# Performance work log

Measured on AMD Instinct MI355X. Metric: run time of the kernel, lower is better.

Reference implementation:

```python
import jax, jax.numpy as jnp
import numpy as np

B, T, E = 8, 1024, 1024
H, HS = 16, 64  # num_heads, head_size; H*HS == E


def setup_inputs() -> dict:
    key = jax.random.key(0)
    k1, k2, k3, k4, k5, k6 = jax.random.split(key, 6)
    x = jax.random.normal(k1, (B, T, E), dtype=jnp.float32)
    s = E ** -0.5
    Wk = jax.random.normal(k2, (H, HS, E), dtype=jnp.float32) * s
    Wq = jax.random.normal(k3, (H, HS, E), dtype=jnp.float32) * s
    Wv = jax.random.normal(k4, (H, HS, E), dtype=jnp.float32) * s
    Wproj = jax.random.normal(k5, (E, E), dtype=jnp.float32) * s
    i = 0
    return {"x": x, "Wk": Wk, "Wq": Wq, "Wv": Wv, "Wproj": Wproj, "i": i}


def reference(x, Wk, Wq, Wv, Wproj, i):
    # choices fixed at full supernet config: embed_dim=E, head_size=HS, no biases.
    b, t, e = x.shape
    hs = Wk.shape[1]
    # per-head projections, heads batched: [B,H,T,HS]
    k = jnp.einsum('bte,hde->bhtd', x, Wk)
    q = jnp.einsum('bte,hde->bhtd', x, Wq)
    v = jnp.einsum('bte,hde->bhtd', x, Wv)
    wei = jnp.einsum('bhtd,bhsd->bhts', q, k) * (hs ** -0.5)  # [B,H,T,T]
    causal = jnp.tril(jnp.ones((t, t), dtype=bool))
    wei = jnp.where(causal, wei, -jnp.inf)
    wei = jax.nn.softmax(wei, axis=-1)  # dropout p=0 (eval)
    out = jnp.einsum('bhts,bhsd->bthd', wei, v).reshape(b, t, -1)  # concat heads
    out = out @ Wproj.T  # proj, bias_proj=False
    return out
```

## Files before the change

### kernel.cpp

```cpp
#include <hip/hip_runtime.h>

#define B_  8
#define T_  1024
#define E_  1024
#define H_  16
#define HS_ 64
#define K_  1024

typedef __bf16 bf16x8 __attribute__((ext_vector_type(8)));
typedef float  f32x4  __attribute__((ext_vector_type(4)));
typedef unsigned short us;

__device__ __forceinline__ us f2bf(float f) {
    union { float f; unsigned int i; } c; c.f = f;
    unsigned int x = c.i;
    return (us)((x + 0x7fff + ((x >> 16) & 1)) >> 16);
}
__device__ __forceinline__ us f2bf_t(float f) {
    union { float f; unsigned int i; } c; c.f = f;
    return (us)(c.i >> 16);
}
__device__ __forceinline__ bf16x8 cvt8(const float* p) {
    float4 a = *reinterpret_cast<const float4*>(p);
    float4 b = *reinterpret_cast<const float4*>(p + 4);
    union { bf16x8 v; us u[8]; } c;
    c.u[0] = f2bf(a.x); c.u[1] = f2bf(a.y); c.u[2] = f2bf(a.z); c.u[3] = f2bf(a.w);
    c.u[4] = f2bf(b.x); c.u[5] = f2bf(b.y); c.u[6] = f2bf(b.z); c.u[7] = f2bf(b.w);
    return c.v;
}
__device__ __forceinline__ void async_cp16(const us* g, us* l) {
    __builtin_amdgcn_global_load_lds((const unsigned int*)g, (unsigned int*)l, 16, 0, 0);
}

__global__ __launch_bounds__(256) void cvt_kernel(
    const float* __restrict__ sx, const float* __restrict__ sq,
    const float* __restrict__ sk, const float* __restrict__ sv,
    const float* __restrict__ sp,
    us* __restrict__ dx, us* __restrict__ dq, us* __restrict__ dk,
    us* __restrict__ dv, us* __restrict__ dp)
{
    const int y = blockIdx.y;
    const float* src = (y == 0) ? sx : (y == 1) ? sq : (y == 2) ? sk : (y == 3) ? sv : sp;
    us*          dst = (y == 0) ? dx : (y == 1) ? dq : (y == 2) ? dk : (y == 3) ? dv : dp;
    const size_t n = (y == 0) ? (size_t)B_ * T_ * E_ : (size_t)E_ * E_;
    const size_t i = ((size_t)blockIdx.x * 256 + threadIdx.x) * 8;
    if (i >= n) return;
    *reinterpret_cast<bf16x8*>(dst + i) = cvt8(src + i);
}

__global__ __launch_bounds__(256) void qkv_gf(
    const us* __restrict__ A,
    const us* __restrict__ Wq, const us* __restrict__ Wk, const us* __restrict__ Wv,
    us* __restrict__ q, us* __restrict__ k, us* __restrict__ vT)
{
    const int type = blockIdx.z;
    const us* Bm = (type == 0) ? Wq : (type == 1) ? Wk : Wv;
    us* out      = (type == 0) ? q  : (type == 1) ? k  : vT;
    const int vtrans = (type == 2);

    __shared__ __align__(16) us As[128 * 64];
    __shared__ __align__(16) us Bs[128 * 64];

    const int tid  = threadIdx.x;
    const int lane = tid & 63;
    const int w    = tid >> 6;
    const int quad = lane >> 4;
    const int l15  = lane & 15;
    const int wm   = w >> 1, wn = w & 1;
    const int row0 = blockIdx.x * 128;
    const int col0 = blockIdx.y * 128;
    const int x7   = l15 & 7;

    f32x4 acc[4][4] = {};
    for (int k0 = 0; k0 < K_; k0 += 64) {
        __syncthreads();
#pragma unroll
        for (int i = 0; i < 4; ++i) {
            const int idx = tid + i * 256;
            const int r   = idx >> 3;
            const int c8  = ((idx & 7) ^ (r & 7)) * 8;
            async_cp16(A  + (size_t)(row0 + r) * K_ + k0 + c8, &As[idx * 8]);
            async_cp16(Bm + (size_t)(col0 + r) * K_ + k0 + c8, &Bs[idx * 8]);
        }
        __syncthreads();
#pragma unroll
        for (int kk = 0; kk < 2; ++kk) {
            const int ca = ((kk * 4 + quad) ^ x7) * 8;
            bf16x8 af[4], bf[4];
#pragma unroll
            for (int t = 0; t < 4; ++t) {
                af[t] = *reinterpret_cast<const bf16x8*>(&As[(wm * 64 + t * 16 + l15) * 64 + ca]);
                bf[t] = *reinterpret_cast<const bf16x8*>(&Bs[(wn * 64 + t * 16 + l15) * 64 + ca]);
            }
#pragma unroll
            for (int mt = 0; mt < 4; ++mt)
#pragma unroll
                for (int nt = 0; nt < 4; ++nt)
                    acc[mt][nt] = __builtin_amdgcn_mfma_f32_16x16x32_bf16(af[mt], bf[nt], acc[mt][nt], 0, 0, 0);
        }
    }

#pragma unroll
    for (int mt = 0; mt < 4; ++mt)
#pragma unroll
        for (int nt = 0; nt < 4; ++nt)
#pragma unroll
            for (int r = 0; r < 4; ++r) {
                const int m = row0 + wm * 64 + mt * 16 + quad * 4 + r;
                const int n = col0 + wn * 64 + nt * 16 + l15;
                const int b = m >> 10, t = m & 1023;
                const int h = n >> 6,  d = n & 63;
                const us vb = f2bf(acc[mt][nt][r]);
                if (vtrans)  out[((size_t)((b * 16 + h) * 64 + d)) * 1024 + t] = vb;
                else         out[((size_t)(b * 16 + h) * 1024 + t) * 64 + d] = vb;
            }
}

__global__ __launch_bounds__(256) void proj_gf(
    const us* __restrict__ A, const us* __restrict__ Bm, float* __restrict__ C)
{
    __shared__ __align__(16) us As[128 * 64];
    __shared__ __align__(16) us Bs[128 * 64];

    const int tid  = threadIdx.x;
    const int lane = tid & 63;
    const int w    = tid >> 6;
    const int quad = lane >> 4;
    const int l15  = lane & 15;
    const int wm   = w >> 1, wn = w & 1;
    const int row0 = blockIdx.x * 128;
    const int col0 = blockIdx.y * 128;
    const int x7   = l15 & 7;

    f32x4 acc[4][4] = {};
    for (int k0 = 0; k0 < K_; k0 += 64) {
        __syncthreads();
#pragma unroll
        for (int i = 0; i < 4; ++i) {
            const int idx = tid + i * 256;
            const int r   = idx >> 3;
            const int c8  = ((idx & 7) ^ (r & 7)) * 8;
            async_cp16(A  + (size_t)(row0 + r) * K_ + k0 + c8, &As[idx * 8]);
            async_cp16(Bm + (size_t)(col0 + r) * K_ + k0 + c8, &Bs[idx * 8]);
        }
        __syncthreads();
#pragma unroll
        for (int kk = 0; kk < 2; ++kk) {
            const int ca = ((kk * 4 + quad) ^ x7) * 8;
            bf16x8 af[4], bf[4];
#pragma unroll
            for (int t = 0; t < 4; ++t) {
                af[t] = *reinterpret_cast<const bf16x8*>(&As[(wm * 64 + t * 16 + l15) * 64 + ca]);
                bf[t] = *reinterpret_cast<const bf16x8*>(&Bs[(wn * 64 + t * 16 + l15) * 64 + ca]);
            }
#pragma unroll
            for (int mt = 0; mt < 4; ++mt)
#pragma unroll
                for (int nt = 0; nt < 4; ++nt)
                    acc[mt][nt] = __builtin_amdgcn_mfma_f32_16x16x32_bf16(af[mt], bf[nt], acc[mt][nt], 0, 0, 0);
        }
    }

#pragma unroll
    for (int mt = 0; mt < 4; ++mt)
#pragma unroll
        for (int nt = 0; nt < 4; ++nt)
#pragma unroll
            for (int r = 0; r < 4; ++r) {
                const int m = row0 + wm * 64 + mt * 16 + quad * 4 + r;
                const int n = col0 + wn * 64 + nt * 16 + l15;
                C[(size_t)m * E_ + n] = acc[mt][nt][r];
            }
}

#define CSCALE 0.18033688011112042f

__device__ __forceinline__ void qk_step_nomax(
    const us (*kt)[72], us (*psw)[72],
    const bf16x8& qf0, const bf16x8& qf1,
    float* lsum,
    int s0, int rowlo, int quad, int l15, bool diag)
{
    f32x4 sacc[4] = {};
#pragma unroll
    for (int nt = 0; nt < 4; ++nt) {
        bf16x8 kf0 = *reinterpret_cast<const bf16x8*>(&kt[nt * 16 + l15][quad * 8]);
        bf16x8 kf1 = *reinterpret_cast<const bf16x8*>(&kt[nt * 16 + l15][quad * 8 + 32]);
        sacc[nt] = __builtin_amdgcn_mfma_f32_16x16x32_bf16(qf0, kf0, sacc[nt], 0, 0, 0);
        sacc[nt] = __builtin_amdgcn_mfma_f32_16x16x32_bf16(qf1, kf1, sacc[nt], 0, 0, 0);
    }
    if (diag) {
#pragma unroll
        for (int nt = 0; nt < 4; ++nt)
#pragma unroll
            for (int r = 0; r < 4; ++r)
                if (s0 + nt * 16 + l15 > rowlo + quad * 4 + r) sacc[nt][r] = -1e30f;
    }
#pragma unroll
    for (int r = 0; r < 4; ++r)
#pragma unroll
        for (int nt = 0; nt < 4; ++nt) {
            const float p = exp2f(sacc[nt][r] * CSCALE);
            lsum[r] += p;
            psw[quad * 4 + r][nt * 16 + l15] = f2bf_t(p);
        }
}

__global__ __launch_bounds__(256) void attn_v6(
    const us* __restrict__ Q, const us* __restrict__ K,
    const us* __restrict__ VT, us* __restrict__ O)
{
    const int px = blockIdx.x;
    const int bh = blockIdx.y;
    const int tA = px, tB = 15 - px;
    const size_t base  = (size_t)bh * T_ * HS_;
    const size_t baseT = (size_t)bh * HS_ * T_;
    const int tid  = threadIdx.x;
    const int w    = tid >> 6;
    const int lane = tid & 63;
    const int quad = lane >> 4;
    const int l15  = lane & 15;

    __shared__ __align__(16) us kt[64][72];
    __shared__ __align__(16) us vt[64][72];
    __shared__ __align__(16) us psA[4][16][72];
    __shared__ __align__(16) us psB[4][16][72];

    const int rowA = tA * 64 + w * 16;
    const int rowB = tB * 64 + w * 16;

    bf16x8 qfA0, qfA1, qfB0, qfB1;
    {
        const us* qa = Q + base + (size_t)(rowA + l15) * HS_ + quad * 8;
        const us* qb = Q + base + (size_t)(rowB + l15) * HS_ + quad * 8;
        qfA0 = *reinterpret_cast<const bf16x8*>(qa);
        qfA1 = *reinterpret_cast<const bf16x8*>(qa + 32);
        qfB0 = *reinterpret_cast<const bf16x8*>(qb);
        qfB1 = *reinterpret_cast<const bf16x8*>(qb + 32);
    }

    float lA[4] = {0.f, 0.f, 0.f, 0.f}, lB[4] = {0.f, 0.f, 0.f, 0.f};
    f32x4 oA[4] = {}, oB[4] = {};

    const int nch = tB + 1;
    for (int ch = 0; ch < nch; ++ch) {
        const int s0 = ch * 64;
        __syncthreads();
#pragma unroll
        for (int i = 0; i < 2; ++i) {
            const int idx = tid + i * 256;
            const int r   = idx >> 3;
            const int c8  = (idx & 7) * 8;
            *reinterpret_cast<bf16x8*>(&kt[r][c8]) =
                *reinterpret_cast<const bf16x8*>(K + base + (size_t)(s0 + r) * HS_ + c8);
            *reinterpret_cast<bf16x8*>(&vt[r][c8]) =
                *reinterpret_cast<const bf16x8*>(VT + baseT + (size_t)r * T_ + s0 + c8);
        }
        __syncthreads();

        const bool actA = (ch <= tA);
        qk_step_nomax(kt, psB[w], qfB0, qfB1, lB, s0, rowB, quad, l15, ch == tB);
        if (actA)
            qk_step_nomax(kt, psA[w], qfA0, qfA1, lA, s0, rowA, quad, l15, ch == tA);

        bf16x8 pfB0 = *reinterpret_cast<const bf16x8*>(&psB[w][l15][quad * 8]);
        bf16x8 pfB1 = *reinterpret_cast<const bf16x8*>(&psB[w][l15][quad * 8 + 32]);
        bf16x8 pfA0, pfA1;
        if (actA) {
            pfA0 = *reinterpret_cast<const bf16x8*>(&psA[w][l15][quad * 8]);
            pfA1 = *reinterpret_cast<const bf16x8*>(&psA[w][l15][quad * 8 + 32]);
        }
#pragma unroll
        for (int dt = 0; dt < 4; ++dt) {
            bf16x8 vf0 = *reinterpret_cast<const bf16x8*>(&vt[dt * 16 + l15][quad * 8]);
            bf16x8 vf1 = *reinterpret_cast<const bf16x8*>(&vt[dt * 16 + l15][quad * 8 + 32]);
            oB[dt] = __builtin_amdgcn_mfma_f32_16x16x32_bf16(pfB0, vf0, oB[dt], 0, 0, 0);
            oB[dt] = __builtin_amdgcn_mfma_f32_16x16x32_bf16(pfB1, vf1, oB[dt], 0, 0, 0);
            if (actA) {
                oA[dt] = __builtin_amdgcn_mfma_f32_16x16x32_bf16(pfA0, vf0, oA[dt], 0, 0, 0);
                oA[dt] = __builtin_amdgcn_mfma_f32_16x16x32_bf16(pfA1, vf1, oA[dt], 0, 0, 0);
            }
        }
    }

#pragma unroll
    for (int r = 0; r < 4; ++r) {
#pragma unroll
        for (int off = 1; off < 16; off <<= 1) {
            lA[r] += __shfl_xor(lA[r], off);
            lB[r] += __shfl_xor(lB[r], off);
        }
    }
    const int b = bh >> 4, h = bh & 15;
#pragma unroll
    for (int r = 0; r < 4; ++r) {
        const float invA = 1.f / lA[r];
        const float invB = 1.f / lB[r];
        const size_t offA = ((size_t)b * T_ + rowA + quad * 4 + r) * E_ + h * HS_;
        const size_t offB = ((size_t)b * T_ + rowB + quad * 4 + r) * E_ + h * HS_;
#pragma unroll
        for (int dt = 0; dt < 4; ++dt) {
            O[offA + dt * 16 + l15] = f2bf(oA[dt][r] * invA);
            O[offB + dt * 16 + l15] = f2bf(oB[dt][r] * invB);
        }
    }
}

extern "C" void kernel_launch(void* const* d_in, const int* in_sizes, int n_in,
                              void* d_out, int out_size, void* d_ws, size_t ws_size,
                              hipStream_t stream) {
    const float* x  = (const float*)d_in[0];
    const float* Wk = (const float*)d_in[1];
    const float* Wq = (const float*)d_in[2];
    const float* Wv = (const float*)d_in[3];
    const float* Wp = (const float*)d_in[4];

    const size_t qe = (size_t)B_ * H_ * T_ * HS_;
    const size_t we = (size_t)E_ * E_;

    us* xb = (us*)d_ws;
    us* wq = xb + qe;
    us* wk = wq + we;
    us* wv = wk + we;
    us* wp = wv + we;
    us* q  = wp + we;
    us* k  = q + qe;
    us* vT = k + qe;
    us* o  = xb;

    cvt_kernel<<<dim3(4096, 5), 256, 0, stream>>>(x, Wq, Wk, Wv, Wp,
                                                  xb, wq, wk, wv, wp);
    qkv_gf<<<dim3(64, 8, 3), 256, 0, stream>>>(xb, wq, wk, wv, q, k, vT);
    attn_v6<<<dim3(8, 128), 256, 0, stream>>>(q, k, vT, o);
    proj_gf<<<dim3(64, 8), 256, 0, stream>>>(o, wp, (float*)d_out);
}
```

Baseline: 255.2 us.

## Load K and V fragments directly from global memory, dropping LDS staging and barriers

The attention kernel no longer stages each 64-row K and V^T chunk through shared memory behind two block-wide barriers. Each wave now reads its MFMA operand fragments straight from global memory, relying on L1/L2 to absorb the reuse across the four waves. The QK step is also inlined so a single K fragment load feeds both the A and B query tiles. This removes the __syncthreads stalls and LDS traffic, but adds redundant global/cache reads (each wave fetches the full K/V chunk) and exposes memory latency without any explicit prefetch.

```diff
diff --git a/kernel.cpp b/kernel.cpp
--- a/kernel.cpp
+++ b/kernel.cpp
@@ -175,38 +175,7 @@
 
 #define CSCALE 0.18033688011112042f
 
-__device__ __forceinline__ void qk_step_nomax(
-    const us (*kt)[72], us (*psw)[72],
-    const bf16x8& qf0, const bf16x8& qf1,
-    float* lsum,
-    int s0, int rowlo, int quad, int l15, bool diag)
-{
-    f32x4 sacc[4] = {};
-#pragma unroll
-    for (int nt = 0; nt < 4; ++nt) {
-        bf16x8 kf0 = *reinterpret_cast<const bf16x8*>(&kt[nt * 16 + l15][quad * 8]);
-        bf16x8 kf1 = *reinterpret_cast<const bf16x8*>(&kt[nt * 16 + l15][quad * 8 + 32]);
-        sacc[nt] = __builtin_amdgcn_mfma_f32_16x16x32_bf16(qf0, kf0, sacc[nt], 0, 0, 0);
-        sacc[nt] = __builtin_amdgcn_mfma_f32_16x16x32_bf16(qf1, kf1, sacc[nt], 0, 0, 0);
-    }
-    if (diag) {
-#pragma unroll
-        for (int nt = 0; nt < 4; ++nt)
-#pragma unroll
-            for (int r = 0; r < 4; ++r)
-                if (s0 + nt * 16 + l15 > rowlo + quad * 4 + r) sacc[nt][r] = -1e30f;
-    }
-#pragma unroll
-    for (int r = 0; r < 4; ++r)
-#pragma unroll
-        for (int nt = 0; nt < 4; ++nt) {
-            const float p = exp2f(sacc[nt][r] * CSCALE);
-            lsum[r] += p;
-            psw[quad * 4 + r][nt * 16 + l15] = f2bf_t(p);
-        }
-}
-
-__global__ __launch_bounds__(256) void attn_v6(
+__global__ __launch_bounds__(256) void attn_v7(
     const us* __restrict__ Q, const us* __restrict__ K,
     const us* __restrict__ VT, us* __restrict__ O)
 {
@@ -221,8 +190,6 @@
     const int quad = lane >> 4;
     const int l15  = lane & 15;
 
-    __shared__ __align__(16) us kt[64][72];
-    __shared__ __align__(16) us vt[64][72];
     __shared__ __align__(16) us psA[4][16][72];
     __shared__ __align__(16) us psB[4][16][72];
 
@@ -245,23 +212,54 @@
     const int nch = tB + 1;
     for (int ch = 0; ch < nch; ++ch) {
         const int s0 = ch * 64;
-        __syncthreads();
-#pragma unroll
-        for (int i = 0; i < 2; ++i) {
-            const int idx = tid + i * 256;
-            const int r   = idx >> 3;
-            const int c8  = (idx & 7) * 8;
-            *reinterpret_cast<bf16x8*>(&kt[r][c8]) =
-                *reinterpret_cast<const bf16x8*>(K + base + (size_t)(s0 + r) * HS_ + c8);
-            *reinterpret_cast<bf16x8*>(&vt[r][c8]) =
-                *reinterpret_cast<const bf16x8*>(VT + baseT + (size_t)r * T_ + s0 + c8);
-        }
-        __syncthreads();
-
         const bool actA = (ch <= tA);
-        qk_step_nomax(kt, psB[w], qfB0, qfB1, lB, s0, rowB, quad, l15, ch == tB);
-        if (actA)
-            qk_step_nomax(kt, psA[w], qfA0, qfA1, lA, s0, rowA, quad, l15, ch == tA);
+
+        f32x4 sA[4] = {}, sB[4] = {};
+#pragma unroll
+        for (int nt = 0; nt < 4; ++nt) {
+            const us* kp = K + base + (size_t)(s0 + nt * 16 + l15) * HS_ + quad * 8;
+            bf16x8 kf0 = *reinterpret_cast<const bf16x8*>(kp);
+            bf16x8 kf1 = *reinterpret_cast<const bf16x8*>(kp + 32);
+            sB[nt] = __builtin_amdgcn_mfma_f32_16x16x32_bf16(qfB0, kf0, sB[nt], 0, 0, 0);
+            sB[nt] = __builtin_amdgcn_mfma_f32_16x16x32_bf16(qfB1, kf1, sB[nt], 0, 0, 0);
+            if (actA) {
+                sA[nt] = __builtin_amdgcn_mfma_f32_16x16x32_bf16(qfA0, kf0, sA[nt], 0, 0, 0);
+                sA[nt] = __builtin_amdgcn_mfma_f32_16x16x32_bf16(qfA1, kf1, sA[nt], 0, 0, 0);
+            }
+        }
+        if (ch == tB) {
+#pragma unroll
+            for (int nt = 0; nt < 4; ++nt)
+#pragma unroll
+                for (int r = 0; r < 4; ++r)
+                    if (s0 + nt * 16 + l15 > rowB + quad * 4 + r) sB[nt][r] = -1e30f;
+        }
+        if (ch == tA) {
+#pragma unroll
+            for (int nt = 0; nt < 4; ++nt)
+#pragma unroll
+                for (int r = 0; r < 4; ++r)
+                    if (s0 + nt * 16 + l15 > rowA + quad * 4 + r) sA[nt][r] = -1e30f;
+        }
+
+#pragma unroll
+        for (int r = 0; r < 4; ++r)
+#pragma unroll
+            for (int nt = 0; nt < 4; ++nt) {
+                const float pB = exp2f(sB[nt][r] * CSCALE);
+                lB[r] += pB;
+                psB[w][quad * 4 + r][nt * 16 + l15] = f2bf_t(pB);
+            }
+        if (actA) {
+#pragma unroll
+            for (int r = 0; r < 4; ++r)
+#pragma unroll
+                for (int nt = 0; nt < 4; ++nt) {
+                    const float pA = exp2f(sA[nt][r] * CSCALE);
+                    lA[r] += pA;
+                    psA[w][quad * 4 + r][nt * 16 + l15] = f2bf_t(pA);
+                }
+        }
 
         bf16x8 pfB0 = *reinterpret_cast<const bf16x8*>(&psB[w][l15][quad * 8]);
         bf16x8 pfB1 = *reinterpret_cast<const bf16x8*>(&psB[w][l15][quad * 8 + 32]);
@@ -270,10 +268,12 @@
             pfA0 = *reinterpret_cast<const bf16x8*>(&psA[w][l15][quad * 8]);
             pfA1 = *reinterpret_cast<const bf16x8*>(&psA[w][l15][quad * 8 + 32]);
         }
+
 #pragma unroll
         for (int dt = 0; dt < 4; ++dt) {
-            bf16x8 vf0 = *reinterpret_cast<const bf16x8*>(&vt[dt * 16 + l15][quad * 8]);
-            bf16x8 vf1 = *reinterpret_cast<const bf16x8*>(&vt[dt * 16 + l15][quad * 8 + 32]);
+            const us* vp = VT + baseT + (size_t)(dt * 16 + l15) * T_ + s0 + quad * 8;
+            bf16x8 vf0 = *reinterpret_cast<const bf16x8*>(vp);
+            bf16x8 vf1 = *reinterpret_cast<const bf16x8*>(vp + 32);
             oB[dt] = __builtin_amdgcn_mfma_f32_16x16x32_bf16(pfB0, vf0, oB[dt], 0, 0, 0);
             oB[dt] = __builtin_amdgcn_mfma_f32_16x16x32_bf16(pfB1, vf1, oB[dt], 0, 0, 0);
             if (actA) {
@@ -331,6 +331,6 @@
     cvt_kernel<<<dim3(4096, 5), 256, 0, stream>>>(x, Wq, Wk, Wv, Wp,
                                                   xb, wq, wk, wv, wp);
     qkv_gf<<<dim3(64, 8, 3), 256, 0, stream>>>(xb, wq, wk, wv, q, k, vT);
-    attn_v6<<<dim3(8, 128), 256, 0, stream>>>(q, k, vT, o);
+    attn_v7<<<dim3(8, 128), 256, 0, stream>>>(q, k, vT, o);
     proj_gf<<<dim3(64, 8), 256, 0, stream>>>(o, wp, (float*)d_out);
 }
```

New measurement: 325.2 us. 1.27x slower.
